# Optimization experiments

Measured on AMD Instinct MI355X. Metric: run time of the kernel, lower is better.

Reference implementation:

```python
import jax, jax.numpy as jnp
import numpy as np

B, S, HID, NH, W = 4, 4096, 768, 12, 128  # batch, seq, hidden, heads, one-sided window
D = HID // NH


def setup_inputs() -> dict:
    key = jax.random.key(0)
    ks = jax.random.split(key, 4)
    sc = 0.02
    return {
        "hidden_states": jax.random.normal(ks[0], (B, S, HID), jnp.float32),
        "Wq": jax.random.normal(ks[1], (HID, HID), jnp.float32) * sc,
        "bq": jnp.zeros((HID,), jnp.float32),
        "Wk": jax.random.normal(ks[2], (HID, HID), jnp.float32) * sc,
        "bk": jnp.zeros((HID,), jnp.float32),
        "Wv": jax.random.normal(ks[3], (HID, HID), jnp.float32) * sc,
        "bv": jnp.zeros((HID,), jnp.float32),
    }


def _heads(x):
    # [B,S,HID] -> [B*NH, S, D]  (matches transpose_for_scores)
    return x.reshape(B, S, NH, D).transpose(0, 2, 1, 3).reshape(B * NH, S, D)


def _windows(x, w):
    # x: [BH, S, D] -> overlapping key/value windows [BH, S//w, 3w, D]
    xp = jnp.pad(x, ((0, 0), (w, w), (0, 0)))
    xc = xp.reshape(x.shape[0], S // w + 2, w, D)
    return jnp.concatenate([xc[:, :-2], xc[:, 1:-1], xc[:, 2:]], axis=2)


def sliding_window_attention(q, k, v, w):
    # q,k,v: [BH, S, D]; banded attention with 2w+1 diagonals, edges masked -inf
    BH = q.shape[0]
    C = S // w
    qc = (q * (1.0 / np.sqrt(D))).reshape(BH, C, w, D)
    kw = _windows(k, w)                                   # [BH,C,3w,D]
    scores_full = jnp.einsum('bcxd,bcyd->bcxy', qc, kw)   # [BH,C,w,3w]
    x = jnp.arange(w)
    off = jnp.arange(2 * w + 1)
    idx = x[:, None] + off[None, :]                       # [w, 2w+1] diag gather index
    scores = jnp.take_along_axis(scores_full, idx[None, None], axis=-1)  # [BH,C,w,2w+1]
    # mask key positions outside [0, S) (== _mask_invalid_locations)
    qpos = jnp.arange(C)[:, None, None] * w + x[:, None]  # [C,w,1]
    kpos = qpos + off[None, None, :] - w                  # [C,w,2w+1]
    valid = (kpos >= 0) & (kpos < S)
    scores = jnp.where(valid[None], scores, -jnp.inf)
    probs = jax.nn.softmax(scores, axis=-1)
    # scatter banded probs back to chunked [w, 3w] layout, then probs @ value windows
    pw = jnp.zeros((BH, C, w, 3 * w), probs.dtype).at[:, :, x[:, None], idx].set(probs)
    vw = _windows(v, w)                                   # [BH,C,3w,D]
    ctx = jnp.einsum('bcxy,bcyd->bcxd', pw, vw)           # [BH,C,w,D]
    return ctx.reshape(BH, S, D)


def reference(hidden_states, Wq, bq, Wk, bk, Wv, bv):
    q = _heads(hidden_states @ Wq.T + bq)
    k = _heads(hidden_states @ Wk.T + bk)
    v = _heads(hidden_states @ Wv.T + bv)
    ctx = sliding_window_attention(q, k, v, W)            # [B*NH, S, D]
    out = ctx.reshape(B, NH, S, D).transpose(0, 2, 1, 3).reshape(B, S, HID)
    return out
```

## Files before the change

kernel.cpp:

```cpp
#include <hip/hip_runtime.h>

#define BQ 4
#define SQ 4096
#define HIDN 768
#define NH 12
#define DH 64
#define BH (BQ * NH)
#define WIN 128
#define MROWS (BQ * SQ)
#define NCOLS (3 * HIDN)
#define KDIM HIDN
#define BHD_ELEMS (BH * SQ * DH)

using bfrag  = __attribute__((ext_vector_type(8))) short;
using f32x4  = __attribute__((ext_vector_type(4))) float;
using f32x16 = __attribute__((ext_vector_type(16))) float;
using us8    = __attribute__((ext_vector_type(8))) unsigned short;

__device__ __forceinline__ unsigned short f2bf(float f) {
  union { float f; unsigned u; } x; x.f = f;
  unsigned r = x.u + 0x7fffu + ((x.u >> 16) & 1u);
  return (unsigned short)(r >> 16);
}
__device__ __forceinline__ unsigned f2bf2(float lo, float hi) {
  return (unsigned)f2bf(lo) | ((unsigned)f2bf(hi) << 16);
}
__device__ __forceinline__ unsigned cvtpk(float lo, float hi) {
  unsigned u;
  asm("v_cvt_pk_bf16_f32 %0, %1, %2" : "=v"(u) : "v"(lo), "v"(hi));
  return u;
}

__device__ __forceinline__ void gload16(const void* g, void* l) {
  __builtin_amdgcn_global_load_lds(
      (const __attribute__((address_space(1))) unsigned int*)g,
      (__attribute__((address_space(3))) unsigned int*)l, 16, 0, 0);
}

#define WBLK (NCOLS * KDIM / 4 / 256)
#define HBLK 2048

__global__ __launch_bounds__(256) void conv_kernel(
    const float* __restrict__ hid,
    const float* __restrict__ Wq, const float* __restrict__ Wk,
    const float* __restrict__ Wv,
    unsigned short* __restrict__ wb, unsigned short* __restrict__ hb)
{
  const int bid = blockIdx.x;
  if (bid < WBLK) {
    int g = (bid * 256 + threadIdx.x) * 4;
    int n = g / KDIM, k = g - n * KDIM;
    int wsel = n / HIDN, nl = n - wsel * HIDN;
    const float* W = (wsel == 0) ? Wq : (wsel == 1) ? Wk : Wv;
    float4 v = *reinterpret_cast<const float4*>(&W[nl * KDIM + k]);
    ushort4 p;
    p.x = f2bf(v.x); p.y = f2bf(v.y); p.z = f2bf(v.z); p.w = f2bf(v.w);
    *reinterpret_cast<ushort4*>(&wb[g]) = p;
  } else {
    const int N8 = MROWS * KDIM / 8;
    for (int idx = (bid - WBLK) * 256 + threadIdx.x; idx < N8; idx += HBLK * 256) {
      const float4* src = reinterpret_cast<const float4*>(hid) + (size_t)idx * 2;
      float4 a = src[0], b = src[1];
      uint4 o;
      o.x = f2bf2(a.x, a.y); o.y = f2bf2(a.z, a.w);
      o.z = f2bf2(b.x, b.y); o.w = f2bf2(b.z, b.w);
      *reinterpret_cast<uint4*>(&hb[(size_t)idx * 8]) = o;
    }
  }
}

#define BM 128
#define BN 128
#define BKK 64

__global__ __launch_bounds__(256) void proj_kernel(
    const unsigned short* __restrict__ hb,
    const unsigned short* __restrict__ wb,
    const float* __restrict__ bq, const float* __restrict__ bk,
    const float* __restrict__ bv,
    unsigned short* __restrict__ qb, unsigned short* __restrict__ kb,
    unsigned short* __restrict__ vb)
{
  __shared__ unsigned short As[BM][BKK];
  __shared__ unsigned short Bs[BN][BKK];

  const int t = threadIdx.x;
  const int id = blockIdx.x;
  const int swz = (id & 7) * (NCOLS * MROWS / (BM * BN) / 8) + (id >> 3);
  const int bx = swz % (NCOLS / BN);
  const int by = swz / (NCOLS / BN);
  const int m0 = by * BM;
  const int n0 = bx * BN;
  const int wsel = bx / 6;
  const float* bias = (wsel == 0) ? bq : (wsel == 1) ? bk : bv;
  const int nloc0 = n0 - wsel * HIDN;

  const int lane = t & 63;
  const int w = t >> 6;
  const int wm = w >> 1, wn = w & 1;
  const int fr = lane & 15, fq = lane >> 4;
  const int xsw = (fr & 7) << 3;

  const int srow = w * 32 + (lane >> 3);
  const int scol = ((lane & 7) * 8) ^ ((lane >> 3) << 3);
  const unsigned short* gA = &hb[(size_t)(m0 + srow) * KDIM + scol];
  const unsigned short* gB = &wb[(size_t)(n0 + srow) * KDIM + scol];

  f32x4 acc[4][4] = {};

  for (int kt = 0; kt < KDIM / BKK; ++kt) {
    const int k0 = kt * BKK;
    __syncthreads();
    #pragma unroll
    for (int i = 0; i < 4; ++i) {
      gload16(gA + k0 + (size_t)(i * 8) * KDIM, &As[w * 32 + i * 8][0]);
      gload16(gB + k0 + (size_t)(i * 8) * KDIM, &Bs[w * 32 + i * 8][0]);
    }
    __syncthreads();
    #pragma unroll
    for (int kk = 0; kk < 2; ++kk) {
      bfrag a[4], b[4];
      #pragma unroll
      for (int i = 0; i < 4; ++i)
        a[i] = *reinterpret_cast<const bfrag*>(&As[wm * 64 + i * 16 + fr][(kk * 32 + fq * 8) ^ xsw]);
      #pragma unroll
      for (int j = 0; j < 4; ++j)
        b[j] = *reinterpret_cast<const bfrag*>(&Bs[wn * 64 + j * 16 + fr][(kk * 32 + fq * 8) ^ xsw]);
      #pragma unroll
      for (int i = 0; i < 4; ++i)
        #pragma unroll
        for (int j = 0; j < 4; ++j)
          acc[i][j] = __builtin_amdgcn_mfma_f32_16x16x32_bf16(b[j], a[i], acc[i][j], 0, 0, 0);
    }
  }

  unsigned short* outb = (wsel == 0) ? qb : (wsel == 1) ? kb : vb;
  const float qscale = (wsel == 0) ? 0.125f * 1.44269504088896f : 1.0f;
  const int b_ = m0 >> 12;
  #pragma unroll
  for (int j = 0; j < 4; ++j) {
    int nl = nloc0 + wn * 64 + j * 16 + fq * 4;
    int h = nl >> 6, d0 = nl & 63;
    float4 bs4 = *reinterpret_cast<const float4*>(&bias[nl]);
    unsigned short* obase = outb + (size_t)(b_ * NH + h) * SQ * DH + d0;
    #pragma unroll
    for (int i = 0; i < 4; ++i) {
      int m = m0 + wm * 64 + i * 16 + fr;
      int srow_ = m & (SQ - 1);
      f32x4 v = acc[i][j];
      uint2 pk;
      pk.x = f2bf2((v[0] + bs4.x) * qscale, (v[1] + bs4.y) * qscale);
      pk.y = f2bf2((v[2] + bs4.z) * qscale, (v[3] + bs4.w) * qscale);
      *reinterpret_cast<uint2*>(&obase[(size_t)srow_ * DH]) = pk;
    }
  }
}

#define VLD 392
#define THR 11.6f

__global__ __launch_bounds__(256, 3) void attn_kernel(
    const unsigned short* __restrict__ qb,
    const unsigned short* __restrict__ kb,
    const unsigned short* __restrict__ vb,
    float* __restrict__ out)
{
  __shared__ unsigned short Vt[DH][VLD];

  const int id = blockIdx.x;
  const int swz = (id & 7) * (BH * SQ / 128 / 8) + (id >> 3);
  const int c = swz & 31;
  const int bh = swz >> 5;
  const int t = threadIdx.x;
  const int lane = t & 63;
  const int w = t >> 6;
  const int b_ = bh / NH, hd = bh - b_ * NH;
  const int qi = lane & 31, h = lane >> 5;

  const unsigned short* Qbh = qb + bh * (SQ * DH);
  const unsigned short* Kbh = kb + bh * (SQ * DH);
  const unsigned short* Vbh = vb + bh * (SQ * DH);

  const int kstart = c * 128 - WIN;

  for (int it = t; it < 48 * 16; it += 256) {
    int dg = it & 15, kg = it >> 4;
    int kr = kstart + kg * 8;
    ushort4 va[8];
    #pragma unroll
    for (int rr = 0; rr < 8; ++rr) {
      int k = kr + rr;
      int kc = k < 0 ? 0 : (k > SQ - 1 ? SQ - 1 : k);
      va[rr] = *reinterpret_cast<const ushort4*>(&Vbh[(size_t)kc * DH + dg * 4]);
    }
    #pragma unroll
    for (int j = 0; j < 4; ++j) {
      us8 row;
      #pragma unroll
      for (int i = 0; i < 8; ++i)
        row[i] = reinterpret_cast<const unsigned short*>(&va[i])[j];
      *reinterpret_cast<us8*>(&Vt[dg * 4 + j][kg * 8]) = row;
    }
  }
  __syncthreads();

  const int q0w = c * 128 + w * 32;
  const int q = q0w + qi;
  const int kw = q0w - WIN;
  bfrag qf[4];
  #pragma unroll
  for (int kk = 0; kk < 4; ++kk)
    qf[kk] = *reinterpret_cast<const bfrag*>(&Qbh[(size_t)q * DH + kk * 16 + h * 8]);

  const int lo = (-q > -WIN) ? -q : -WIN;
  const int hi = (SQ - 1 - q < WIN) ? (SQ - 1 - q) : WIN;
  const int hq = 4 * h - qi;
  const bool edge = (c == 0) || (c == 31);

  f32x16 c0 = {}, c1 = {};
  float m = -3e38f, ls = 0.f;

  bfrag kf[4];
  {
    int krow = kw + qi;
    int kc = krow < 0 ? 0 : (krow > SQ - 1 ? SQ - 1 : krow);
    #pragma unroll
    for (int kk = 0; kk < 4; ++kk)
      kf[kk] = *reinterpret_cast<const bfrag*>(&Kbh[(size_t)kc * DH + kk * 16 + h * 8]);
  }

  for (int kt = 0; kt < 9; ++kt) {
    bfrag kfn[4];
    if (kt < 8) {
      int krow = kw + (kt + 1) * 32 + qi;
      int kc = krow < 0 ? 0 : (krow > SQ - 1 ? SQ - 1 : krow);
      #pragma unroll
      for (int kk = 0; kk < 4; ++kk)
        kfn[kk] = *reinterpret_cast<const bfrag*>(&Kbh[(size_t)kc * DH + kk * 16 + h * 8]);
    }

    f32x16 D = {};
    __builtin_amdgcn_s_setprio(1);
    #pragma unroll
    for (int kk = 0; kk < 4; ++kk)
      D = __builtin_amdgcn_mfma_f32_32x32x16_bf16(kf[kk], qf[kk], D, 0, 0, 0);
    __builtin_amdgcn_s_setprio(0);

    if (edge || kt == 0 || kt == 8) {
      #pragma unroll
      for (int r = 0; r < 16; ++r) {
        int klocal = (r & 3) + 8 * (r >> 2);
        int dk = kt * 32 + klocal - WIN + hq;
        if (dk < lo || dk > hi) D[r] = -1e30f;
      }
    }

    float pm = D[0];
    #pragma unroll
    for (int r = 1; r < 16; ++r) pm = fmaxf(pm, D[r]);
    pm = fmaxf(pm, __shfl_xor(pm, 32));

    if (!__all(pm <= m + THR)) {
      float mn = fmaxf(m, pm);
      float al = __builtin_amdgcn_exp2f(m - mn);
      #pragma unroll
      for (int r = 0; r < 16; ++r) {
        float av = __shfl(al, (r & 3) + 8 * (r >> 2) + 4 * h);
        c0[r] *= av; c1[r] *= av;
      }
      ls *= al;
      m = mn;
    }

    float p[16];
    float sum = 0.f;
    #pragma unroll
    for (int r = 0; r < 16; ++r) {
      p[r] = __builtin_amdgcn_exp2f(D[r] - m);
      sum += p[r];
    }
    ls += sum;

    unsigned U[8];
    #pragma unroll
    for (int g = 0; g < 8; ++g) U[g] = cvtpk(p[2 * g], p[2 * g + 1]);

    unsigned f0[4], f1[4];
    {
      unsigned x, y, xs, ys;
      x = U[0]; y = U[2]; xs = __shfl_xor(x, 32); ys = __shfl_xor(y, 32);
      f0[0] = h ? ys : x;  f0[2] = h ? y : xs;
      x = U[1]; y = U[3]; xs = __shfl_xor(x, 32); ys = __shfl_xor(y, 32);
      f0[1] = h ? ys : x;  f0[3] = h ? y : xs;
      x = U[4]; y = U[6]; xs = __shfl_xor(x, 32); ys = __shfl_xor(y, 32);
      f1[0] = h ? ys : x;  f1[2] = h ? y : xs;
      x = U[5]; y = U[7]; xs = __shfl_xor(x, 32); ys = __shfl_xor(y, 32);
      f1[1] = h ? ys : x;  f1[3] = h ? y : xs;
    }

    const int colbase = w * 32 + kt * 32;
    bfrag paA, paB;
    {
      uint4 ua = {f0[0], f0[1], f0[2], f0[3]};
      uint4 ub = {f1[0], f1[1], f1[2], f1[3]};
      paA = *reinterpret_cast<bfrag*>(&ua);
      paB = *reinterpret_cast<bfrag*>(&ub);
    }
    bfrag v00 = *reinterpret_cast<const bfrag*>(&Vt[qi][colbase + h * 8]);
    bfrag v01 = *reinterpret_cast<const bfrag*>(&Vt[32 + qi][colbase + h * 8]);
    bfrag v10 = *reinterpret_cast<const bfrag*>(&Vt[qi][colbase + 16 + h * 8]);
    bfrag v11 = *reinterpret_cast<const bfrag*>(&Vt[32 + qi][colbase + 16 + h * 8]);
    __builtin_amdgcn_s_setprio(1);
    c0 = __builtin_amdgcn_mfma_f32_32x32x16_bf16(paA, v00, c0, 0, 0, 0);
    c1 = __builtin_amdgcn_mfma_f32_32x32x16_bf16(paA, v01, c1, 0, 0, 0);
    c0 = __builtin_amdgcn_mfma_f32_32x32x16_bf16(paB, v10, c0, 0, 0, 0);
    c1 = __builtin_amdgcn_mfma_f32_32x32x16_bf16(paB, v11, c1, 0, 0, 0);
    __builtin_amdgcn_s_setprio(0);

    #pragma unroll
    for (int kk = 0; kk < 4; ++kk) kf[kk] = kfn[kk];
  }

  float lt = ls + __shfl_xor(ls, 32);
  float rinv = 1.0f / lt;
  #pragma unroll
  for (int r = 0; r < 16; ++r) {
    int qrow = (r & 3) + 8 * (r >> 2) + 4 * h;
    float rv = __shfl(rinv, qrow);
    size_t obase = (size_t)(b_ * SQ + q0w + qrow) * HIDN + hd * DH;
    out[obase + qi] = c0[r] * rv;
    out[obase + 32 + qi] = c1[r] * rv;
  }
}

extern "C" void kernel_launch(void* const* d_in, const int* in_sizes, int n_in,
                              void* d_out, int out_size, void* d_ws, size_t ws_size,
                              hipStream_t stream) {
  const float* hid = (const float*)d_in[0];
  const float* Wq  = (const float*)d_in[1];
  const float* bq  = (const float*)d_in[2];
  const float* Wk  = (const float*)d_in[3];
  const float* bk  = (const float*)d_in[4];
  const float* Wv  = (const float*)d_in[5];
  const float* bv  = (const float*)d_in[6];
  float* out = (float*)d_out;

  unsigned short* qb = (unsigned short*)d_ws;
  unsigned short* kb = qb + BHD_ELEMS;
  unsigned short* vb = kb + BHD_ELEMS;
  unsigned short* wb = vb + BHD_ELEMS;
  unsigned short* hb = wb + NCOLS * KDIM;

  conv_kernel<<<dim3(WBLK + HBLK), dim3(256), 0, stream>>>(hid, Wq, Wk, Wv, wb, hb);

  dim3 g1(NCOLS * MROWS / (BM * BN));
  proj_kernel<<<g1, dim3(256), 0, stream>>>(hb, wb, bq, bk, bv, qb, kb, vb);

  dim3 g2(BH * SQ / 128);
  attn_kernel<<<g2, dim3(256), 0, stream>>>(qb, kb, vb, out);
}
```

Before: 143.2 us.

## Double-buffer projection GEMM LDS tiles with a smaller K step

```diff
diff --git a/kernel.cpp b/kernel.cpp
--- a/kernel.cpp
+++ b/kernel.cpp
@@ -71,7 +71,8 @@
 
 #define BM 128
 #define BN 128
-#define BKK 64
+#define BKK 32
+#define NKT (KDIM / BKK)
 
 __global__ __launch_bounds__(256) void proj_kernel(
     const unsigned short* __restrict__ hb,
@@ -81,8 +82,8 @@
     unsigned short* __restrict__ qb, unsigned short* __restrict__ kb,
     unsigned short* __restrict__ vb)
 {
-  __shared__ unsigned short As[BM][BKK];
-  __shared__ unsigned short Bs[BN][BKK];
+  __shared__ unsigned short As[2][BM][BKK];
+  __shared__ unsigned short Bs[2][BN][BKK];
 
   const int t = threadIdx.x;
   const int id = blockIdx.x;
@@ -99,39 +100,44 @@
   const int w = t >> 6;
   const int wm = w >> 1, wn = w & 1;
   const int fr = lane & 15, fq = lane >> 4;
-  const int xsw = (fr & 7) << 3;
-
-  const int srow = w * 32 + (lane >> 3);
-  const int scol = ((lane & 7) * 8) ^ ((lane >> 3) << 3);
+
+  const int srow = w * 32 + (lane >> 2);
+  const int scol = (lane & 3) * 8;
   const unsigned short* gA = &hb[(size_t)(m0 + srow) * KDIM + scol];
   const unsigned short* gB = &wb[(size_t)(n0 + srow) * KDIM + scol];
 
   f32x4 acc[4][4] = {};
 
-  for (int kt = 0; kt < KDIM / BKK; ++kt) {
-    const int k0 = kt * BKK;
+  {
+    gload16(gA, &As[0][w * 32][0]);
+    gload16(gA + (size_t)16 * KDIM, &As[0][w * 32 + 16][0]);
+    gload16(gB, &Bs[0][w * 32][0]);
+    gload16(gB + (size_t)16 * KDIM, &Bs[0][w * 32 + 16][0]);
+  }
+  __syncthreads();
+
+  for (int kt = 0; kt < NKT; ++kt) {
+    const int cb = kt & 1;
+    if (kt < NKT - 1) {
+      const int k1 = (kt + 1) * BKK;
+      gload16(gA + k1, &As[cb ^ 1][w * 32][0]);
+      gload16(gA + k1 + (size_t)16 * KDIM, &As[cb ^ 1][w * 32 + 16][0]);
+      gload16(gB + k1, &Bs[cb ^ 1][w * 32][0]);
+      gload16(gB + k1 + (size_t)16 * KDIM, &Bs[cb ^ 1][w * 32 + 16][0]);
+    }
+    bfrag a[4], b[4];
+    #pragma unroll
+    for (int i = 0; i < 4; ++i)
+      a[i] = *reinterpret_cast<const bfrag*>(&As[cb][wm * 64 + i * 16 + fr][fq * 8]);
+    #pragma unroll
+    for (int j = 0; j < 4; ++j)
+      b[j] = *reinterpret_cast<const bfrag*>(&Bs[cb][wn * 64 + j * 16 + fr][fq * 8]);
+    #pragma unroll
+    for (int i = 0; i < 4; ++i)
+      #pragma unroll
+      for (int j = 0; j < 4; ++j)
+        acc[i][j] = __builtin_amdgcn_mfma_f32_16x16x32_bf16(b[j], a[i], acc[i][j], 0, 0, 0);
     __syncthreads();
-    #pragma unroll
-    for (int i = 0; i < 4; ++i) {
-      gload16(gA + k0 + (size_t)(i * 8) * KDIM, &As[w * 32 + i * 8][0]);
-      gload16(gB + k0 + (size_t)(i * 8) * KDIM, &Bs[w * 32 + i * 8][0]);
-    }
-    __syncthreads();
-    #pragma unroll
-    for (int kk = 0; kk < 2; ++kk) {
-      bfrag a[4], b[4];
-      #pragma unroll
-      for (int i = 0; i < 4; ++i)
-        a[i] = *reinterpret_cast<const bfrag*>(&As[wm * 64 + i * 16 + fr][(kk * 32 + fq * 8) ^ xsw]);
-      #pragma unroll
-      for (int j = 0; j < 4; ++j)
-        b[j] = *reinterpret_cast<const bfrag*>(&Bs[wn * 64 + j * 16 + fr][(kk * 32 + fq * 8) ^ xsw]);
-      #pragma unroll
-      for (int i = 0; i < 4; ++i)
-        #pragma unroll
-        for (int j = 0; j < 4; ++j)
-          acc[i][j] = __builtin_amdgcn_mfma_f32_16x16x32_bf16(b[j], a[i], acc[i][j], 0, 0, 0);
-    }
   }
 
   unsigned short* outb = (wsel == 0) ? qb : (wsel == 1) ? kb : vb;
```

After: 152.7 us. 1.07x slower.
